# Kernel optimization log

Measured on AMD Instinct MI355X. Metric: run time of the kernel, lower is better.

The kernel has to match this reference:

```python
import jax, jax.numpy as jnp
import numpy as np

N, L, D = 8, 2048, 128


def setup_inputs() -> dict:
    key = jax.random.key(0)
    k1, k2, k3, k4 = jax.random.split(key, 4)
    x_t = jax.random.normal(k1, (N, L, D), jnp.float32)
    x_f = jax.random.normal(k2, (N, L, D), jnp.float32)
    W = jax.random.normal(k3, (D, D), jnp.float32) / np.sqrt(D)  # proj weight (torch Linear layout)
    b = jax.random.normal(k4, (D,), jnp.float32) * 0.02
    return {"x_t": x_t, "x_f": x_f, "W": W, "b": b}


def _col_score(a, c, scale):
    # softmax attention with zeroed diagonal, then column-sum -> [N, L]
    att = jnp.einsum('nld,nmd->nlm', a, c) * scale
    att = jax.nn.softmax(att, axis=-1)
    att = att * (1.0 - jnp.eye(att.shape[-1], dtype=att.dtype))
    return jnp.sum(att, axis=1)


def _mask(score, time):
    # score: [N, L]; k-th extreme threshold, k = L//2
    k = int(0.5 * score.shape[1])
    if time:
        vals, _ = jax.lax.top_k(score, k)          # k largest, descending
        theta = vals[:, -1:]                        # k-th largest
        return score > theta
    else:
        vals, _ = jax.lax.top_k(-score, k)          # k smallest
        theta = -vals[:, -1:]                       # k-th smallest
        return score <= theta


def reference(x_t, x_f, W, b):
    scale = 1.0 / np.sqrt(W.shape[0])
    pt = x_t @ W.T + b
    pf = x_f @ W.T + b
    score_t = _col_score(pt, pt, scale)
    score_f = _col_score(pf, pf, scale)
    score_tf = _col_score(pt, pf, scale)
    score_ft = _col_score(pf, pt, scale)
    mask_t = _mask(score_t, False)
    mask_f = _mask(score_f, False)
    mask_tf = _mask(score_tf, True)   # computed in original forward (unused in blend)
    mask_ft = _mask(score_ft, True)
    mask_t1 = (mask_t & ~mask_f)[:, :, None]   # [N, L, 1] broadcast over D
    mask_f1 = (mask_f & ~mask_t)[:, :, None]
    x_t1 = jnp.where(mask_t1, x_f, x_t)
    x_f1 = jnp.where(mask_f1, x_t, x_f)
    return (0.5 * (x_t1 + x_t), 0.5 * (x_f1 + x_f))
```

## Files before the change

### kernel.cpp

```cpp
#include <hip/hip_runtime.h>
#include <math.h>

#define LL 2048
#define DD 128
#define NS 16
#define SLAB (LL * DD)
#define SCALE 0.08838834764831845f
#define NT 16

typedef __attribute__((ext_vector_type(8))) short short8v;
typedef __attribute__((ext_vector_type(4))) float float4v;

__device__ __forceinline__ unsigned int f2bf(float f) {
    unsigned int u = __float_as_uint(f);
    u += 0x7fffu + ((u >> 16) & 1u);
    return u >> 16;
}

__device__ __forceinline__ void strip_decode(int bx, int by, int& ib, int& ns) {
    const int lin = by * 16 + bx;
    const int xcd = lin & 7;
    const int w   = lin >> 3;
    ns = xcd + 8 * (w & 1);
    ib = w >> 1;
}

__device__ __forceinline__ void gl_lds16(const void* g, void* l) {
    __builtin_amdgcn_global_load_lds(
        (const __attribute__((address_space(1))) void*)g,
        (__attribute__((address_space(3))) void*)l, 16, 0, 0);
}

__device__ __forceinline__ void stage512(
    const unsigned short* __restrict__ gT, unsigned short* lbuf, int tid)
{
    const int row = tid >> 2;
    const int oc  = (tid & 3) ^ ((row >> 1) & 3);
    const int sb  = tid & ~63;
    gl_lds16(gT + (size_t)row * DD + oc * 8, lbuf + (size_t)sb * 8);
}

#define PSYNC(N) do { __builtin_amdgcn_sched_barrier(0); \
    asm volatile("s_waitcnt vmcnt(" #N ")" ::: "memory"); \
    __builtin_amdgcn_s_barrier(); \
    __builtin_amdgcn_sched_barrier(0); } while (0)

#define KCSTEP(kc, SH, SL, DO_STAGE)                                          \
  { if (DO_STAGE) {                                                           \
        stage512((SH), pan[2 * (((kc) + 2) & 3)],     tid);                   \
        stage512((SL), pan[2 * (((kc) + 2) & 3) + 1], tid);                   \
    }                                                                         \
    const unsigned short* BhP = pan[2 * (kc)];                                \
    const unsigned short* BlP = pan[2 * (kc) + 1];                            \
    short8v bh[2], bl[2];                                                     \
    _Pragma("unroll")                                                         \
    for (int ct = 0; ct < 2; ++ct) {                                          \
        const int r = wc * 32 + ct * 16 + l16;                                \
        const int off = r * 32 + ((quad ^ ((r >> 1) & 3)) << 3);              \
        bh[ct] = *(const short8v*)&BhP[off];                                  \
        bl[ct] = *(const short8v*)&BlP[off];                                  \
    }                                                                         \
    __builtin_amdgcn_s_setprio(1);                                            \
    _Pragma("unroll")                                                         \
    for (int rt = 0; rt < 4; ++rt)                                            \
    _Pragma("unroll")                                                         \
    for (int ct = 0; ct < 2; ++ct) {                                          \
        acc[rt][ct] = __builtin_amdgcn_mfma_f32_16x16x32_bf16(ah[kc][rt], bh[ct], acc[rt][ct], 0, 0, 0); \
        acc[rt][ct] = __builtin_amdgcn_mfma_f32_16x16x32_bf16(ah[kc][rt], bl[ct], acc[rt][ct], 0, 0, 0); \
        acc[rt][ct] = __builtin_amdgcn_mfma_f32_16x16x32_bf16(al[kc][rt], bh[ct], acc[rt][ct], 0, 0, 0); \
    }                                                                         \
    __builtin_amdgcn_s_setprio(0); }

__global__ __launch_bounds__(256, 4) void proj_kernel(
    const float* __restrict__ xt, const float* __restrict__ xf,
    const float* __restrict__ W,  const float* __restrict__ bias,
    unsigned short* __restrict__ Ph, unsigned short* __restrict__ Pl)
{
    __shared__ float Alds[64 * 36];
    __shared__ float Blds[128 * 36];
    __shared__ float bs[128];
    const int ns = blockIdx.y;
    const int l0 = blockIdx.x * 64;
    const int src = ns >> 3, n = ns & 7;
    const float* x = (src ? xf : xt) + (size_t)n * LL * DD;
    const int tid = threadIdx.x;
    const int ty = tid >> 4, tx = tid & 15;

    if (tid < 128) bs[tid] = bias[tid];
    __syncthreads();

    float acc[4][8];
#pragma unroll
    for (int i = 0; i < 4; ++i)
#pragma unroll
        for (int j = 0; j < 8; ++j) acc[i][j] = bs[tx + 16 * j];

    for (int kc = 0; kc < 4; ++kc) {
        __syncthreads();
#pragma unroll
        for (int t = 0; t < 2; ++t) {
            int idx = tid + t * 256;
            int r = idx >> 3, k4 = (idx & 7) << 2;
            *(float4*)&Alds[r * 36 + k4] =
                *(const float4*)&x[(size_t)(l0 + r) * DD + kc * 32 + k4];
        }
#pragma unroll
        for (int t = 0; t < 4; ++t) {
            int idx = tid + t * 256;
            int r = idx >> 3, k4 = (idx & 7) << 2;
            *(float4*)&Blds[r * 36 + k4] =
                *(const float4*)&W[(size_t)r * DD + kc * 32 + k4];
        }
        __syncthreads();
#pragma unroll
        for (int k4 = 0; k4 < 32; k4 += 4) {
            float4 a4[4], b4[8];
#pragma unroll
            for (int i = 0; i < 4; ++i) a4[i] = *(const float4*)&Alds[(ty + 16 * i) * 36 + k4];
#pragma unroll
            for (int j = 0; j < 8; ++j) b4[j] = *(const float4*)&Blds[(tx + 16 * j) * 36 + k4];
#pragma unroll
            for (int i = 0; i < 4; ++i)
#pragma unroll
                for (int j = 0; j < 8; ++j) {
                    acc[i][j] = fmaf(a4[i].x, b4[j].x, acc[i][j]);
                    acc[i][j] = fmaf(a4[i].y, b4[j].y, acc[i][j]);
                    acc[i][j] = fmaf(a4[i].z, b4[j].z, acc[i][j]);
                    acc[i][j] = fmaf(a4[i].w, b4[j].w, acc[i][j]);
                }
        }
    }
#pragma unroll
    for (int i = 0; i < 4; ++i) {
        const size_t rowo = (size_t)ns * SLAB + (size_t)(l0 + ty + 16 * i) * DD;
#pragma unroll
        for (int j = 0; j < 8; ++j) {
            float p = acc[i][j];
            unsigned int hb = f2bf(p);
            float hf = __uint_as_float(hb << 16);
            unsigned int lb = f2bf(p - hf);
            Ph[rowo + tx + 16 * j] = (unsigned short)hb;
            Pl[rowo + tx + 16 * j] = (unsigned short)lb;
        }
    }
}

__global__ __launch_bounds__(512, 2) void stats_kernel(
    const unsigned short* __restrict__ Ph, const unsigned short* __restrict__ Pl,
    float* __restrict__ iZfin)
{
    __shared__ unsigned short pan[8][4096];
    __shared__ float zl[128][4];
    int ib, ns;  strip_decode(blockIdx.x, blockIdx.y, ib, ns);
    const int tid = threadIdx.x;
    const int lane = tid & 63, quad = lane >> 4, l16 = lane & 15, wave = tid >> 6;
    const int wr = wave >> 2, wc = wave & 3;

    const unsigned short* sAh = Ph + (size_t)ns * SLAB + (size_t)ib * 128 * DD;
    const unsigned short* sAl = Pl + (size_t)ns * SLAB + (size_t)ib * 128 * DD;
    const unsigned short* sBh = Ph + (size_t)ns * SLAB;
    const unsigned short* sBl = Pl + (size_t)ns * SLAB;

    short8v ah[4][4], al[4][4];
#pragma unroll
    for (int kc = 0; kc < 4; ++kc)
#pragma unroll
        for (int rt = 0; rt < 4; ++rt) {
            const size_t o = (size_t)(wr * 64 + rt * 16 + l16) * DD + kc * 32 + quad * 8;
            ah[kc][rt] = *(const short8v*)&sAh[o];
            al[kc][rt] = *(const short8v*)&sAl[o];
        }
    stage512(sBh,      pan[0], tid);
    stage512(sBl,      pan[1], tid);
    stage512(sBh + 32, pan[2], tid);
    stage512(sBl + 32, pan[3], tid);
    PSYNC(2);

    float z[4][4];
#pragma unroll
    for (int rt = 0; rt < 4; ++rt)
#pragma unroll
        for (int rg = 0; rg < 4; ++rg) z[rt][rg] = 0.f;

    const unsigned short* bJh = sBh;
    const unsigned short* bJl = sBl;
#pragma unroll 1
    for (int jb = 0; jb < 16; ++jb) {
        float4v acc[4][2];
#pragma unroll
        for (int rt = 0; rt < 4; ++rt)
#pragma unroll
            for (int ct = 0; ct < 2; ++ct)
#pragma unroll
                for (int r = 0; r < 4; ++r) acc[rt][ct][r] = 0.f;

        const unsigned short* nJh = bJh + 128 * DD;
        const unsigned short* nJl = bJl + 128 * DD;
        const bool more = (jb < 15);

        KCSTEP(0, bJh + 64, bJl + 64, true);  PSYNC(2);
        KCSTEP(1, bJh + 96, bJl + 96, true);  PSYNC(2);
        KCSTEP(2, nJh,      nJl,      more);
        if (more) PSYNC(2); else PSYNC(0);
        KCSTEP(3, nJh + 32, nJl + 32, more);

#pragma unroll
        for (int rt = 0; rt < 4; ++rt)
#pragma unroll
            for (int rg = 0; rg < 4; ++rg) {
                float e0 = __expf(acc[rt][0][rg] * SCALE);
                float e1 = __expf(acc[rt][1][rg] * SCALE);
                z[rt][rg] += e0 + e1;
            }
        if (more) PSYNC(2);
        bJh = nJh;  bJl = nJl;
    }

#pragma unroll
    for (int rt = 0; rt < 4; ++rt)
#pragma unroll
        for (int rg = 0; rg < 4; ++rg) {
            float s = z[rt][rg];
            s += __shfl_xor(s, 1);
            s += __shfl_xor(s, 2);
            s += __shfl_xor(s, 4);
            s += __shfl_xor(s, 8);
            z[rt][rg] = s;
        }
    if (l16 == 0) {
#pragma unroll
        for (int rt = 0; rt < 4; ++rt)
#pragma unroll
            for (int rg = 0; rg < 4; ++rg)
                zl[wr * 64 + rt * 16 + quad * 4 + rg][wc] = z[rt][rg];
    }
    __syncthreads();
    if (tid < 128) {
        float Z = zl[tid][0] + zl[tid][1] + zl[tid][2] + zl[tid][3];
        iZfin[ns * LL + ib * 128 + tid] = 1.0f / Z;
    }
}

__global__ __launch_bounds__(512, 2) void colsum_kernel(
    const unsigned short* __restrict__ Ph, const unsigned short* __restrict__ Pl,
    const float* __restrict__ iZfin, float* __restrict__ Spart)
{
    __shared__ unsigned short pan[8][4096];
    __shared__ float scs[2048][2];
    int ib, ns;  strip_decode(blockIdx.x, blockIdx.y, ib, ns);
    const int tid = threadIdx.x;
    const int lane = tid & 63, quad = lane >> 4, l16 = lane & 15, wave = tid >> 6;
    const int wr = wave >> 2, wc = wave & 3;

    const unsigned short* sAh = Ph + (size_t)ns * SLAB + (size_t)ib * 128 * DD;
    const unsigned short* sAl = Pl + (size_t)ns * SLAB + (size_t)ib * 128 * DD;
    const unsigned short* sBh = Ph + (size_t)ns * SLAB;
    const unsigned short* sBl = Pl + (size_t)ns * SLAB;

    float wrow[4][4];
#pragma unroll
    for (int rt = 0; rt < 4; ++rt)
#pragma unroll
        for (int rg = 0; rg < 4; ++rg)
            wrow[rt][rg] = iZfin[ns * LL + ib * 128 + wr * 64 + rt * 16 + quad * 4 + rg];

    short8v ah[4][4], al[4][4];
#pragma unroll
    for (int kc = 0; kc < 4; ++kc)
#pragma unroll
        for (int rt = 0; rt < 4; ++rt) {
            const size_t o = (size_t)(wr * 64 + rt * 16 + l16) * DD + kc * 32 + quad * 8;
            ah[kc][rt] = *(const short8v*)&sAh[o];
            al[kc][rt] = *(const short8v*)&sAl[o];
        }
    stage512(sBh,      pan[0], tid);
    stage512(sBl,      pan[1], tid);
    stage512(sBh + 32, pan[2], tid);
    stage512(sBl + 32, pan[3], tid);
    PSYNC(2);

    const unsigned short* bJh = sBh;
    const unsigned short* bJl = sBl;
#pragma unroll 1
    for (int jb = 0; jb < 16; ++jb) {
        float4v acc[4][2];
#pragma unroll
        for (int rt = 0; rt < 4; ++rt)
#pragma unroll
            for (int ct = 0; ct < 2; ++ct)
#pragma unroll
                for (int r = 0; r < 4; ++r) acc[rt][ct][r] = 0.f;

        const unsigned short* nJh = bJh + 128 * DD;
        const unsigned short* nJl = bJl + 128 * DD;
        const bool more = (jb < 15);

        KCSTEP(0, bJh + 64, bJl + 64, true);  PSYNC(2);
        KCSTEP(1, bJh + 96, bJl + 96, true);  PSYNC(2);
        KCSTEP(2, nJh,      nJl,      more);
        if (more) PSYNC(2); else PSYNC(0);
        KCSTEP(3, nJh + 32, nJl + 32, more);

        float colp0 = 0.f, colp1 = 0.f;
        const bool dgj = (jb == ib);
#pragma unroll
        for (int rt = 0; rt < 4; ++rt)
#pragma unroll
            for (int rg = 0; rg < 4; ++rg) {
                const int rl = wr * 64 + rt * 16 + quad * 4 + rg;
                float e0 = __expf(acc[rt][0][rg] * SCALE);
                float e1 = __expf(acc[rt][1][rg] * SCALE);
                bool s0 = dgj && (rl == wc * 32 + l16);
                bool s1 = dgj && (rl == wc * 32 + 16 + l16);
                colp0 += s0 ? 0.f : e0 * wrow[rt][rg];
                colp1 += s1 ? 0.f : e1 * wrow[rt][rg];
            }
        colp0 += __shfl_xor(colp0, 16);
        colp0 += __shfl_xor(colp0, 32);
        colp1 += __shfl_xor(colp1, 16);
        colp1 += __shfl_xor(colp1, 32);
        if (quad == 0) {
            scs[jb * 128 + wc * 32 + l16][wr]      = colp0;
            scs[jb * 128 + wc * 32 + 16 + l16][wr] = colp1;
        }
        if (more) PSYNC(2);
        bJh = nJh;  bJl = nJl;
    }

    __syncthreads();
#pragma unroll
    for (int g = 0; g < 4; ++g) {
        const int m = tid + g * 512;
        Spart[((size_t)ns * LL + m) * 16 + ib] = scs[m][0] + scs[m][1];
    }
}

__global__ __launch_bounds__(1024) void mask_kernel(
    const float* __restrict__ Spart, unsigned char* __restrict__ maskbuf)
{
    __shared__ double s[LL];
    const int ns = blockIdx.x;
    const int half = blockIdx.y;
    const int tid = threadIdx.x;
#pragma unroll
    for (int h = 0; h < 2; ++h) {
        int m = tid + h * 1024;
        const float* sp = Spart + ((size_t)ns * LL + m) * 16;
        double a = 0.0;
#pragma unroll
        for (int t = 0; t < 16; ++t) a += (double)sp[t];
        s[m] = a;
    }
    __syncthreads();
    const int i = half * 1024 + tid;
    const double si = s[i];
    int cnt = 0;
    for (int j = 0; j < LL; ++j) cnt += (s[j] < si) ? 1 : 0;
    maskbuf[ns * LL + i] = (cnt < 1024) ? 1 : 0;
}

__global__ __launch_bounds__(256) void blend_kernel(
    const float* __restrict__ xt, const float* __restrict__ xf,
    const unsigned char* __restrict__ maskbuf, float* __restrict__ out)
{
    const int idx4 = blockIdx.x * 256 + threadIdx.x;
    const size_t q = (size_t)idx4 * 4;
    const int row = (int)(q >> 7);
    const float4 a = *(const float4*)(xt + q);
    const float4 b = *(const float4*)(xf + q);
    const int mt = maskbuf[row] & 1;
    const int mf = maskbuf[16384 + row] & 1;
    const bool ct = mt && !mf;
    const bool cf = mf && !mt;
    float4 av;
    av.x = 0.5f * (a.x + b.x);  av.y = 0.5f * (a.y + b.y);
    av.z = 0.5f * (a.z + b.z);  av.w = 0.5f * (a.w + b.w);
    float4 o0 = ct ? av : a;
    float4 o1 = cf ? av : b;
    *(float4*)(out + q)                   = o0;
    *(float4*)(out + (size_t)2097152 + q) = o1;
}

extern "C" void kernel_launch(void* const* d_in, const int* in_sizes, int n_in,
                              void* d_out, int out_size, void* d_ws, size_t ws_size,
                              hipStream_t stream)
{
    const float* xt = (const float*)d_in[0];
    const float* xf = (const float*)d_in[1];
    const float* W  = (const float*)d_in[2];
    const float* b  = (const float*)d_in[3];
    float* out = (float*)d_out;

    unsigned short* Ph = (unsigned short*)d_out;
    unsigned short* Pl = Ph + (size_t)NS * SLAB;

    float* iZfin = (float*)d_ws;
    float* Spart = iZfin + NS * LL;
    unsigned char* maskbuf = (unsigned char*)(Spart + (size_t)16 * LL * 16);

    proj_kernel<<<dim3(32, NS), 256, 0, stream>>>(xt, xf, W, b, Ph, Pl);
    stats_kernel<<<dim3(16, 16), 512, 0, stream>>>(Ph, Pl, iZfin);
    colsum_kernel<<<dim3(16, 16), 512, 0, stream>>>(Ph, Pl, iZfin, Spart);
    mask_kernel<<<dim3(NS, 2), 1024, 0, stream>>>(Spart, maskbuf);
    blend_kernel<<<2048, 256, 0, stream>>>(xt, xf, maskbuf, out);
}
```

Baseline: 243.6 us.

## Fuse row-stats and column-sum passes into one score kernel with software pipelining

Merges the stats and colsum kernels into one kernel that computes row normalizers and then column sums in the same block, so one launch and the global iZ round-trip go away. The A-low operand is now staged in LDS instead of held in registers. The inner loop double-buffers the LDS panels and alternates two accumulator sets, so the exp epilogue of one tile overlaps the MFMAs of the next. The cost is more LDS per block (panels, Alpan and scs together), which may limit occupancy, and the loop now uses full __syncthreads instead of the vmcnt-based partial waits.

```diff
diff --git a/kernel.cpp b/kernel.cpp
--- a/kernel.cpp
+++ b/kernel.cpp
@@ -6,7 +6,6 @@
 #define NS 16
 #define SLAB (LL * DD)
 #define SCALE 0.08838834764831845f
-#define NT 16
 
 typedef __attribute__((ext_vector_type(8))) short short8v;
 typedef __attribute__((ext_vector_type(4))) float float4v;
@@ -40,19 +39,21 @@
     gl_lds16(gT + (size_t)row * DD + oc * 8, lbuf + (size_t)sb * 8);
 }
 
-#define PSYNC(N) do { __builtin_amdgcn_sched_barrier(0); \
-    asm volatile("s_waitcnt vmcnt(" #N ")" ::: "memory"); \
-    __builtin_amdgcn_s_barrier(); \
-    __builtin_amdgcn_sched_barrier(0); } while (0)
-
-#define KCSTEP(kc, SH, SL, DO_STAGE)                                          \
-  { if (DO_STAGE) {                                                           \
-        stage512((SH), pan[2 * (((kc) + 2) & 3)],     tid);                   \
-        stage512((SL), pan[2 * (((kc) + 2) & 3) + 1], tid);                   \
-    }                                                                         \
-    const unsigned short* BhP = pan[2 * (kc)];                                \
-    const unsigned short* BlP = pan[2 * (kc) + 1];                            \
-    short8v bh[2], bl[2];                                                     \
+#define STAGE_HALF(DST, GH, GL, KC) do {                       \
+    stage512((GH) + (KC) * 32,       (DST)[0], tid);           \
+    stage512((GL) + (KC) * 32,       (DST)[1], tid);           \
+    stage512((GH) + ((KC) + 1) * 32, (DST)[2], tid);           \
+    stage512((GL) + ((KC) + 1) * 32, (DST)[3], tid); } while (0)
+
+#define ZEROACC(ACC) do {                                      \
+    _Pragma("unroll") for (int rt = 0; rt < 4; ++rt)           \
+    _Pragma("unroll") for (int ct = 0; ct < 2; ++ct)           \
+    _Pragma("unroll") for (int r = 0; r < 4; ++r) (ACC)[rt][ct][r] = 0.f; } while (0)
+
+#define KC2(ACC, CB, KI, AKC) do {                                            \
+    const unsigned short* BhP = (CB)[2 * (KI)];                               \
+    const unsigned short* BlP = (CB)[2 * (KI) + 1];                           \
+    short8v bh[2], bl[2], alv[4];                                             \
     _Pragma("unroll")                                                         \
     for (int ct = 0; ct < 2; ++ct) {                                          \
         const int r = wc * 32 + ct * 16 + l16;                                \
@@ -60,16 +61,47 @@
         bh[ct] = *(const short8v*)&BhP[off];                                  \
         bl[ct] = *(const short8v*)&BlP[off];                                  \
     }                                                                         \
+    _Pragma("unroll")                                                         \
+    for (int rt = 0; rt < 4; ++rt) {                                          \
+        const int r = wr * 64 + rt * 16 + l16;                                \
+        const int off = r * 32 + ((quad ^ ((r >> 1) & 3)) << 3);              \
+        alv[rt] = *(const short8v*)&Alpan[AKC][off];                          \
+    }                                                                         \
     __builtin_amdgcn_s_setprio(1);                                            \
     _Pragma("unroll")                                                         \
     for (int rt = 0; rt < 4; ++rt)                                            \
     _Pragma("unroll")                                                         \
     for (int ct = 0; ct < 2; ++ct) {                                          \
-        acc[rt][ct] = __builtin_amdgcn_mfma_f32_16x16x32_bf16(ah[kc][rt], bh[ct], acc[rt][ct], 0, 0, 0); \
-        acc[rt][ct] = __builtin_amdgcn_mfma_f32_16x16x32_bf16(ah[kc][rt], bl[ct], acc[rt][ct], 0, 0, 0); \
-        acc[rt][ct] = __builtin_amdgcn_mfma_f32_16x16x32_bf16(al[kc][rt], bh[ct], acc[rt][ct], 0, 0, 0); \
+        (ACC)[rt][ct] = __builtin_amdgcn_mfma_f32_16x16x32_bf16(ah[AKC][rt], bh[ct], (ACC)[rt][ct], 0, 0, 0); \
+        (ACC)[rt][ct] = __builtin_amdgcn_mfma_f32_16x16x32_bf16(ah[AKC][rt], bl[ct], (ACC)[rt][ct], 0, 0, 0); \
+        (ACC)[rt][ct] = __builtin_amdgcn_mfma_f32_16x16x32_bf16(alv[rt],     bh[ct], (ACC)[rt][ct], 0, 0, 0); \
     }                                                                         \
-    __builtin_amdgcn_s_setprio(0); }
+    __builtin_amdgcn_s_setprio(0); } while (0)
+
+#define EPI1(ACC) do {                                         \
+    _Pragma("unroll") for (int rt = 0; rt < 4; ++rt)           \
+    _Pragma("unroll") for (int rg = 0; rg < 4; ++rg) {         \
+        float e0 = __expf((ACC)[rt][0][rg] * SCALE);           \
+        float e1 = __expf((ACC)[rt][1][rg] * SCALE);           \
+        z[rt][rg] += e0 + e1; } } while (0)
+
+#define EPI2(ACC, JBV) do {                                    \
+    float colp0 = 0.f, colp1 = 0.f;                            \
+    const bool dgj = ((JBV) == ib);                            \
+    _Pragma("unroll") for (int rt = 0; rt < 4; ++rt)           \
+    _Pragma("unroll") for (int rg = 0; rg < 4; ++rg) {         \
+        const int rl = wr * 64 + rt * 16 + quad * 4 + rg;      \
+        float e0 = __expf((ACC)[rt][0][rg] * SCALE);           \
+        float e1 = __expf((ACC)[rt][1][rg] * SCALE);           \
+        bool s0 = dgj && (rl == wc * 32 + l16);                \
+        bool s1 = dgj && (rl == wc * 32 + 16 + l16);           \
+        colp0 += s0 ? 0.f : e0 * wrow[rt][rg];                 \
+        colp1 += s1 ? 0.f : e1 * wrow[rt][rg]; }               \
+    colp0 += __shfl_xor(colp0, 16); colp0 += __shfl_xor(colp0, 32); \
+    colp1 += __shfl_xor(colp1, 16); colp1 += __shfl_xor(colp1, 32); \
+    if (quad == 0) {                                           \
+        scs[(JBV) * 128 + wc * 32 + l16][wr]      = colp0;     \
+        scs[(JBV) * 128 + wc * 32 + 16 + l16][wr] = colp1; } } while (0)
 
 __global__ __launch_bounds__(256, 4) void proj_kernel(
     const float* __restrict__ xt, const float* __restrict__ xf,
@@ -145,11 +177,13 @@
     }
 }
 
-__global__ __launch_bounds__(512, 2) void stats_kernel(
+__global__ __launch_bounds__(512, 2) void score_kernel(
     const unsigned short* __restrict__ Ph, const unsigned short* __restrict__ Pl,
-    float* __restrict__ iZfin)
-{
-    __shared__ unsigned short pan[8][4096];
+    float* __restrict__ Spart)
+{
+    __shared__ unsigned short pan[2][4][4096];
+    __shared__ unsigned short Alpan[4][4096];
+    __shared__ float scs[2048][2];
     __shared__ float zl[128][4];
     int ib, ns;  strip_decode(blockIdx.x, blockIdx.y, ib, ns);
     const int tid = threadIdx.x;
@@ -161,60 +195,61 @@
     const unsigned short* sBh = Ph + (size_t)ns * SLAB;
     const unsigned short* sBl = Pl + (size_t)ns * SLAB;
 
-    short8v ah[4][4], al[4][4];
+    stage512(sAl,      Alpan[0], tid);
+    stage512(sAl + 32, Alpan[1], tid);
+    stage512(sAl + 64, Alpan[2], tid);
+    stage512(sAl + 96, Alpan[3], tid);
+    STAGE_HALF(pan[0], sBh, sBl, 0);
+    short8v ah[4][4];
 #pragma unroll
     for (int kc = 0; kc < 4; ++kc)
 #pragma unroll
-        for (int rt = 0; rt < 4; ++rt) {
-            const size_t o = (size_t)(wr * 64 + rt * 16 + l16) * DD + kc * 32 + quad * 8;
-            ah[kc][rt] = *(const short8v*)&sAh[o];
-            al[kc][rt] = *(const short8v*)&sAl[o];
-        }
-    stage512(sBh,      pan[0], tid);
-    stage512(sBl,      pan[1], tid);
-    stage512(sBh + 32, pan[2], tid);
-    stage512(sBl + 32, pan[3], tid);
-    PSYNC(2);
-
+        for (int rt = 0; rt < 4; ++rt)
+            ah[kc][rt] = *(const short8v*)
+                &sAh[(size_t)(wr * 64 + rt * 16 + l16) * DD + kc * 32 + quad * 8];
+    __syncthreads();
+
+    float4v accA[4][2], accB[4][2];
     float z[4][4];
 #pragma unroll
     for (int rt = 0; rt < 4; ++rt)
 #pragma unroll
         for (int rg = 0; rg < 4; ++rg) z[rt][rg] = 0.f;
 
-    const unsigned short* bJh = sBh;
-    const unsigned short* bJl = sBl;
 #pragma unroll 1
-    for (int jb = 0; jb < 16; ++jb) {
-        float4v acc[4][2];
-#pragma unroll
-        for (int rt = 0; rt < 4; ++rt)
-#pragma unroll
-            for (int ct = 0; ct < 2; ++ct)
-#pragma unroll
-                for (int r = 0; r < 4; ++r) acc[rt][ct][r] = 0.f;
-
-        const unsigned short* nJh = bJh + 128 * DD;
-        const unsigned short* nJl = bJl + 128 * DD;
-        const bool more = (jb < 15);
-
-        KCSTEP(0, bJh + 64, bJl + 64, true);  PSYNC(2);
-        KCSTEP(1, bJh + 96, bJl + 96, true);  PSYNC(2);
-        KCSTEP(2, nJh,      nJl,      more);
-        if (more) PSYNC(2); else PSYNC(0);
-        KCSTEP(3, nJh + 32, nJl + 32, more);
-
-#pragma unroll
-        for (int rt = 0; rt < 4; ++rt)
-#pragma unroll
-            for (int rg = 0; rg < 4; ++rg) {
-                float e0 = __expf(acc[rt][0][rg] * SCALE);
-                float e1 = __expf(acc[rt][1][rg] * SCALE);
-                z[rt][rg] += e0 + e1;
-            }
-        if (more) PSYNC(2);
-        bJh = nJh;  bJl = nJl;
-    }
+    for (int jp = 0; jp < 8; ++jp) {
+        const unsigned short* b0h = sBh + (size_t)(2 * jp) * 128 * DD;
+        const unsigned short* b0l = sBl + (size_t)(2 * jp) * 128 * DD;
+        const unsigned short* b1h = b0h + 128 * DD;
+        const unsigned short* b1l = b0l + 128 * DD;
+        const unsigned short* b2h = b1h + 128 * DD;
+        const unsigned short* b2l = b1l + 128 * DD;
+
+        ZEROACC(accA);
+        STAGE_HALF(pan[1], b0h, b0l, 2);
+        KC2(accA, pan[0], 0, 0);
+        KC2(accA, pan[0], 1, 1);
+        if (jp) EPI1(accB);
+        __syncthreads();
+
+        STAGE_HALF(pan[0], b1h, b1l, 0);
+        KC2(accA, pan[1], 0, 2);
+        KC2(accA, pan[1], 1, 3);
+        __syncthreads();
+
+        ZEROACC(accB);
+        STAGE_HALF(pan[1], b1h, b1l, 2);
+        KC2(accB, pan[0], 0, 0);
+        KC2(accB, pan[0], 1, 1);
+        EPI1(accA);
+        __syncthreads();
+
+        if (jp < 7) STAGE_HALF(pan[0], b2h, b2l, 0);
+        KC2(accB, pan[1], 0, 2);
+        KC2(accB, pan[1], 1, 3);
+        __syncthreads();
+    }
+    EPI1(accB);
 
 #pragma unroll
     for (int rt = 0; rt < 4; ++rt)
@@ -225,107 +260,53 @@
             s += __shfl_xor(s, 2);
             s += __shfl_xor(s, 4);
             s += __shfl_xor(s, 8);
-            z[rt][rg] = s;
-        }
-    if (l16 == 0) {
-#pragma unroll
-        for (int rt = 0; rt < 4; ++rt)
-#pragma unroll
-            for (int rg = 0; rg < 4; ++rg)
-                zl[wr * 64 + rt * 16 + quad * 4 + rg][wc] = z[rt][rg];
-    }
-    __syncthreads();
-    if (tid < 128) {
-        float Z = zl[tid][0] + zl[tid][1] + zl[tid][2] + zl[tid][3];
-        iZfin[ns * LL + ib * 128 + tid] = 1.0f / Z;
-    }
-}
-
-__global__ __launch_bounds__(512, 2) void colsum_kernel(
-    const unsigned short* __restrict__ Ph, const unsigned short* __restrict__ Pl,
-    const float* __restrict__ iZfin, float* __restrict__ Spart)
-{
-    __shared__ unsigned short pan[8][4096];
-    __shared__ float scs[2048][2];
-    int ib, ns;  strip_decode(blockIdx.x, blockIdx.y, ib, ns);
-    const int tid = threadIdx.x;
-    const int lane = tid & 63, quad = lane >> 4, l16 = lane & 15, wave = tid >> 6;
-    const int wr = wave >> 2, wc = wave & 3;
-
-    const unsigned short* sAh = Ph + (size_t)ns * SLAB + (size_t)ib * 128 * DD;
-    const unsigned short* sAl = Pl + (size_t)ns * SLAB + (size_t)ib * 128 * DD;
-    const unsigned short* sBh = Ph + (size_t)ns * SLAB;
-    const unsigned short* sBl = Pl + (size_t)ns * SLAB;
-
+            if (l16 == 0) zl[wr * 64 + rt * 16 + quad * 4 + rg][wc] = s;
+        }
+    STAGE_HALF(pan[0], sBh, sBl, 0);
+    __syncthreads();
     float wrow[4][4];
 #pragma unroll
     for (int rt = 0; rt < 4; ++rt)
 #pragma unroll
-        for (int rg = 0; rg < 4; ++rg)
-            wrow[rt][rg] = iZfin[ns * LL + ib * 128 + wr * 64 + rt * 16 + quad * 4 + rg];
-
-    short8v ah[4][4], al[4][4];
-#pragma unroll
-    for (int kc = 0; kc < 4; ++kc)
-#pragma unroll
-        for (int rt = 0; rt < 4; ++rt) {
-            const size_t o = (size_t)(wr * 64 + rt * 16 + l16) * DD + kc * 32 + quad * 8;
-            ah[kc][rt] = *(const short8v*)&sAh[o];
-            al[kc][rt] = *(const short8v*)&sAl[o];
-        }
-    stage512(sBh,      pan[0], tid);
-    stage512(sBl,      pan[1], tid);
-    stage512(sBh + 32, pan[2], tid);
-    stage512(sBl + 32, pan[3], tid);
-    PSYNC(2);
-
-    const unsigned short* bJh = sBh;
-    const unsigned short* bJl = sBl;
+        for (int rg = 0; rg < 4; ++rg) {
+            const int row = wr * 64 + rt * 16 + quad * 4 + rg;
+            wrow[rt][rg] = 1.0f / (zl[row][0] + zl[row][1] + zl[row][2] + zl[row][3]);
+        }
+
 #pragma unroll 1
-    for (int jb = 0; jb < 16; ++jb) {
-        float4v acc[4][2];
-#pragma unroll
-        for (int rt = 0; rt < 4; ++rt)
-#pragma unroll
-            for (int ct = 0; ct < 2; ++ct)
-#pragma unroll
-                for (int r = 0; r < 4; ++r) acc[rt][ct][r] = 0.f;
-
-        const unsigned short* nJh = bJh + 128 * DD;
-        const unsigned short* nJl = bJl + 128 * DD;
-        const bool more = (jb < 15);
-
-        KCSTEP(0, bJh + 64, bJl + 64, true);  PSYNC(2);
-        KCSTEP(1, bJh + 96, bJl + 96, true);  PSYNC(2);
-        KCSTEP(2, nJh,      nJl,      more);
-        if (more) PSYNC(2); else PSYNC(0);
-        KCSTEP(3, nJh + 32, nJl + 32, more);
-
-        float colp0 = 0.f, colp1 = 0.f;
-        const bool dgj = (jb == ib);
-#pragma unroll
-        for (int rt = 0; rt < 4; ++rt)
-#pragma unroll
-            for (int rg = 0; rg < 4; ++rg) {
-                const int rl = wr * 64 + rt * 16 + quad * 4 + rg;
-                float e0 = __expf(acc[rt][0][rg] * SCALE);
-                float e1 = __expf(acc[rt][1][rg] * SCALE);
-                bool s0 = dgj && (rl == wc * 32 + l16);
-                bool s1 = dgj && (rl == wc * 32 + 16 + l16);
-                colp0 += s0 ? 0.f : e0 * wrow[rt][rg];
-                colp1 += s1 ? 0.f : e1 * wrow[rt][rg];
-            }
-        colp0 += __shfl_xor(colp0, 16);
-        colp0 += __shfl_xor(colp0, 32);
-        colp1 += __shfl_xor(colp1, 16);
-        colp1 += __shfl_xor(colp1, 32);
-        if (quad == 0) {
-            scs[jb * 128 + wc * 32 + l16][wr]      = colp0;
-            scs[jb * 128 + wc * 32 + 16 + l16][wr] = colp1;
-        }
-        if (more) PSYNC(2);
-        bJh = nJh;  bJl = nJl;
-    }
+    for (int jp = 0; jp < 8; ++jp) {
+        const unsigned short* b0h = sBh + (size_t)(2 * jp) * 128 * DD;
+        const unsigned short* b0l = sBl + (size_t)(2 * jp) * 128 * DD;
+        const unsigned short* b1h = b0h + 128 * DD;
+        const unsigned short* b1l = b0l + 128 * DD;
+        const unsigned short* b2h = b1h + 128 * DD;
+        const unsigned short* b2l = b1l + 128 * DD;
+
+        ZEROACC(accA);
+        STAGE_HALF(pan[1], b0h, b0l, 2);
+        KC2(accA, pan[0], 0, 0);
+        KC2(accA, pan[0], 1, 1);
+        if (jp) EPI2(accB, 2 * jp - 1);
+        __syncthreads();
+
+        STAGE_HALF(pan[0], b1h, b1l, 0);
+        KC2(accA, pan[1], 0, 2);
+        KC2(accA, pan[1], 1, 3);
+        __syncthreads();
+
+        ZEROACC(accB);
+        STAGE_HALF(pan[1], b1h, b1l, 2);
+        KC2(accB, pan[0], 0, 0);
+        KC2(accB, pan[0], 1, 1);
+        EPI2(accA, 2 * jp);
+        __syncthreads();
+
+        if (jp < 7) STAGE_HALF(pan[0], b2h, b2l, 0);
+        KC2(accB, pan[1], 0, 2);
+        KC2(accB, pan[1], 1, 3);
+        __syncthreads();
+    }
+    EPI2(accB, 15);
 
     __syncthreads();
 #pragma unroll
@@ -394,13 +375,11 @@
     unsigned short* Ph = (unsigned short*)d_out;
     unsigned short* Pl = Ph + (size_t)NS * SLAB;
 
-    float* iZfin = (float*)d_ws;
-    float* Spart = iZfin + NS * LL;
+    float* Spart = (float*)d_ws;
     unsigned char* maskbuf = (unsigned char*)(Spart + (size_t)16 * LL * 16);
 
     proj_kernel<<<dim3(32, NS), 256, 0, stream>>>(xt, xf, W, b, Ph, Pl);
-    stats_kernel<<<dim3(16, 16), 512, 0, stream>>>(Ph, Pl, iZfin);
-    colsum_kernel<<<dim3(16, 16), 512, 0, stream>>>(Ph, Pl, iZfin, Spart);
+    score_kernel<<<dim3(16, 16), 512, 0, stream>>>(Ph, Pl, Spart);
     mask_kernel<<<dim3(NS, 2), 1024, 0, stream>>>(Spart, maskbuf);
     blend_kernel<<<2048, 256, 0, stream>>>(xt, xf, maskbuf, out);
 }
```

After: 237.8 us. -2.4%, faster.
